# Optimization experiments

Measured on AMD Instinct MI355X. Metric: run time of the kernel, lower is better.

The kernel has to match this reference:

```python
import jax, jax.numpy as jnp
import numpy as np

B, Nc, Ns, Nz, Nx, K = 2, 128, 2048, 256, 256, 4


def setup_inputs() -> dict:
    key = jax.random.key(0)
    k1, k2, k3 = jax.random.split(key, 3)
    # RF channel data: [B, Nc, Ns, K]
    rf = jax.random.normal(k1, (B, Nc, Ns, K), dtype=jnp.float32)
    # Imaging grid point coordinates (meters), ~4 cm field: [B, Nz, Nx, 3]
    g = jax.random.uniform(k2, (B, Nz, Nx, 3), dtype=jnp.float32) * 0.04
    # Receiver element positions (meters): [B, Nc, 3]
    pr = jax.random.uniform(k3, (B, Nc, 3), dtype=jnp.float32) * 0.04
    # Acquisition params per batch: [c0 (m/s), fs (Hz), t0 (s), unused]
    p = jnp.tile(jnp.array([1540.0, 40.0e6, 0.0, 0.0], dtype=jnp.float32), (B, 1))
    return {"rf": rf, "g": g, "pr": pr, "p": p}


def reference(rf, g, pr, p):
    # rf: [B, Nc, Ns, K]; g: [B, Nz, Nx, 3]; pr: [B, Nc, 3]; p: [B, 4]
    b, nc, ns, k = rf.shape
    nz, nx = g.shape[1], g.shape[2]
    m = nz * nx

    c0 = p[:, 0][:, None, None, None]
    fs = p[:, 1][:, None, None, None]
    t0 = p[:, 2][:, None, None, None]

    d_tx = g[..., 2]  # [B, Nz, Nx] transmit path = depth coordinate
    # receive path: distance from each receiver to each pixel -> [B, Nc, Nz, Nx]
    d_rx = jnp.linalg.norm(g[:, None, :, :, :] - pr[:, :, None, None, :], axis=-1)
    # fractional sample index of the round-trip delay
    samples = fs * (t0 + (d_rx + d_tx[:, None, :, :])) / c0  # [B, Nc, Nz, Nx]
    s = samples.reshape(b, nc, m)

    # batch_interp_regular_1d_grid with x_ref_min=0, x_ref_max=Ns-1 on Ns points
    # -> unit grid spacing, constant extension (clamp) outside the grid.
    s = jnp.clip(s, 0.0, float(ns - 1))
    i0 = jnp.clip(jnp.floor(s).astype(jnp.int32), 0, ns - 2)  # [B, Nc, M]
    w = (s - i0.astype(s.dtype))[..., None]                   # [B, Nc, M, 1]

    idx0 = jnp.broadcast_to(i0[..., None], (b, nc, m, k))
    y0 = jnp.take_along_axis(rf, idx0, axis=2)      # [B, Nc, M, K]
    y1 = jnp.take_along_axis(rf, idx0 + 1, axis=2)  # [B, Nc, M, K]
    interp = y0 * (1.0 - w) + y1 * w

    # delay-and-sum over channels, then back to image layout [B, Nz, Nx, K]
    y_das = jnp.sum(interp, axis=1).reshape(b, nz, nx, k)
    return y_das
```

## Files before the change

kernel.cpp:

```cpp
#include <hip/hip_runtime.h>


#define NBATCH 2
#define NC 128
#define NS 2048
#define NK 4
#define NM 65536

#define THREADS 1024
#define PX_PER_THREAD 2
#define PX_PER_BLOCK (THREADS * PX_PER_THREAD)
#define C_PER_BLOCK 16
#define N_CHUNKS (NC / C_PER_BLOCK)
#define N_TILES (NM / PX_PER_BLOCK)
#define NBLOCKS (NBATCH * N_TILES * N_CHUNKS)
#define SLICE_F4 (NS * NK / 4)

#define PART_BYTES ((size_t)N_CHUNKS * NBATCH * NM * NK * 4)

__device__ __forceinline__ void stage_channel(const float* slice, float4* lbuf, int t) {
#pragma unroll
    for (int r = 0; r < SLICE_F4 / THREADS; ++r) {
        const int d = r * THREADS + t;
        __builtin_amdgcn_global_load_lds(
            (const __attribute__((address_space(1))) void*)(slice + (size_t)d * 4),
            (__attribute__((address_space(3))) void*)(lbuf + d),
            16, 0, 0);
    }
}

template <bool ATOMIC>
__global__ __launch_bounds__(THREADS, 8) void das_kernel(
    const float* __restrict__ rf, const float* __restrict__ g,
    const float* __restrict__ pr, const float* __restrict__ p,
    float* __restrict__ dst)
{
    __shared__ float4 sbuf[2][SLICE_F4];

    const int bid   = blockIdx.x;
    const int chunk = bid & (N_CHUNKS - 1);
    const int tile  = (bid >> 3) & (N_TILES - 1);
    const int b     = bid >> 8;
    const int t     = threadIdx.x;
    const int px0   = tile * PX_PER_BLOCK;

    const float c0v = p[b * 4 + 0];
    const float fsv = p[b * 4 + 1];
    const float t0v = p[b * 4 + 2];
    const float scale = fsv / c0v;
    const float sb0   = scale * t0v;

    float gx[PX_PER_THREAD], gy[PX_PER_THREAD], gzv[PX_PER_THREAD], sbase[PX_PER_THREAD];
#pragma unroll
    for (int j = 0; j < PX_PER_THREAD; ++j) {
        const int m = px0 + j * THREADS + t;
        const float* gp = g + ((size_t)b * NM + m) * 3;
        gx[j]  = gp[0];
        gy[j]  = gp[1];
        gzv[j] = gp[2];
        sbase[j] = sb0 + scale * gzv[j];
    }

    float4 acc[PX_PER_THREAD];
#pragma unroll
    for (int j = 0; j < PX_PER_THREAD; ++j) acc[j] = make_float4(0.f, 0.f, 0.f, 0.f);

    const int ch0 = chunk * C_PER_BLOCK;
    const float* slice0 = rf + (size_t)(b * NC + ch0) * NS * NK;

    stage_channel(slice0, &sbuf[0][0], t);

    for (int cc = 0; cc < C_PER_BLOCK; ++cc) {
        __syncthreads();
        if (cc + 1 < C_PER_BLOCK)
            stage_channel(slice0 + (size_t)(cc + 1) * NS * NK,
                          &sbuf[(cc + 1) & 1][0], t);

        const float4* lb = &sbuf[cc & 1][0];
        const float* prp = pr + ((size_t)(b * NC + ch0 + cc)) * 3;
        const float prx = prp[0], pry = prp[1], prz = prp[2];

#pragma unroll
        for (int j = 0; j < PX_PER_THREAD; ++j) {
            const float dx = gx[j]  - prx;
            const float dy = gy[j]  - pry;
            const float dz = gzv[j] - prz;
            const float drx = __builtin_amdgcn_sqrtf(fmaf(dx, dx, fmaf(dy, dy, dz * dz)));
            float s = fmaf(scale, drx, sbase[j]);
            s = fminf(fmaxf(s, 0.0f), (float)(NS - 1));
            const float fi = fminf(floorf(s), (float)(NS - 2));
            const float w  = s - fi;
            const float wm = 1.0f - w;
            const int i0 = (int)fi;
            const float4 y0 = lb[i0];
            const float4 y1 = lb[i0 + 1];
            acc[j].x = fmaf(y0.x, wm, fmaf(y1.x, w, acc[j].x));
            acc[j].y = fmaf(y0.y, wm, fmaf(y1.y, w, acc[j].y));
            acc[j].z = fmaf(y0.z, wm, fmaf(y1.z, w, acc[j].z));
            acc[j].w = fmaf(y0.w, wm, fmaf(y1.w, w, acc[j].w));
        }
    }

    if (ATOMIC) {
        float* ob = dst + (size_t)b * NM * NK;
#pragma unroll
        for (int j = 0; j < PX_PER_THREAD; ++j) {
            const int m = px0 + j * THREADS + t;
            float* op = ob + (size_t)m * NK;
            atomicAdd(op + 0, acc[j].x);
            atomicAdd(op + 1, acc[j].y);
            atomicAdd(op + 2, acc[j].z);
            atomicAdd(op + 3, acc[j].w);
        }
    } else {
        float4* pw = (float4*)dst + (size_t)(chunk * NBATCH + b) * NM;
#pragma unroll
        for (int j = 0; j < PX_PER_THREAD; ++j) {
            const int m = px0 + j * THREADS + t;
            pw[m] = acc[j];
        }
    }
}

__global__ __launch_bounds__(256) void reduce_kernel(
    const float4* __restrict__ part, float4* __restrict__ out)
{
    const int i = blockIdx.x * 256 + threadIdx.x;
    const size_t stride = (size_t)NBATCH * NM;
    float4 a = part[i];
#pragma unroll
    for (int c = 1; c < N_CHUNKS; ++c) {
        const float4 v = part[c * stride + i];
        a.x += v.x; a.y += v.y; a.z += v.z; a.w += v.w;
    }
    out[i] = a;
}

extern "C" void kernel_launch(void* const* d_in, const int* in_sizes, int n_in,
                              void* d_out, int out_size, void* d_ws, size_t ws_size,
                              hipStream_t stream) {
    (void)in_sizes; (void)n_in;
    const float* rf = (const float*)d_in[0];
    const float* g  = (const float*)d_in[1];
    const float* pr = (const float*)d_in[2];
    const float* p  = (const float*)d_in[3];
    float* out = (float*)d_out;

    if (ws_size >= PART_BYTES) {
        das_kernel<false><<<NBLOCKS, THREADS, 0, stream>>>(rf, g, pr, p, (float*)d_ws);
        reduce_kernel<<<(NBATCH * NM) / 256, 256, 0, stream>>>((const float4*)d_ws,
                                                               (float4*)out);
    } else {
        hipMemsetAsync(d_out, 0, (size_t)out_size * sizeof(float), stream);
        das_kernel<true><<<NBLOCKS, THREADS, 0, stream>>>(rf, g, pr, p, out);
    }
}
```

Before: 87.05 us.

## Stage RF slabs in LDS as fp16, two channels per phase, register-prefetched

Replaces the direct global-to-LDS async copies of fp32 channel slices with register loads that convert to fp16 and store two channels per LDS buffer. Each phase processes two channels between barriers, and the next slab is prefetched into registers during compute. This halves LDS footprint per channel and barrier count, and aims for smaller LDS reads. It adds conversion work and register pressure, and fp16 storage reduces precision of the RF samples, which may exceed tolerance.

Result: slower. 272.3 us (+212.8%).

```diff
diff --git a/kernel.cpp b/kernel.cpp
--- a/kernel.cpp
+++ b/kernel.cpp
@@ -14,18 +14,37 @@
 #define N_CHUNKS (NC / C_PER_BLOCK)
 #define N_TILES (NM / PX_PER_BLOCK)
 #define NBLOCKS (NBATCH * N_TILES * N_CHUNKS)
-#define SLICE_F4 (NS * NK / 4)
+
+#define CH_PER_PHASE 2
+#define N_PHASES (C_PER_BLOCK / CH_PER_PHASE)
+#define SLAB_F4 (CH_PER_PHASE * NS * NK / 4)
+#define SLAB_H  (CH_PER_PHASE * NS * NK)
+#define CH_H    (NS * NK)
 
 #define PART_BYTES ((size_t)N_CHUNKS * NBATCH * NM * NK * 4)
 
-__device__ __forceinline__ void stage_channel(const float* slice, float4* lbuf, int t) {
+typedef __attribute__((ext_vector_type(4))) _Float16 half4;
+typedef __attribute__((ext_vector_type(8))) _Float16 half8;
+
+__device__ __forceinline__ void load_slab(const float* slab, float4* f, int t) {
+    const float4* src = (const float4*)slab;
+    f[0] = src[2 * t];
+    f[1] = src[2 * t + 1];
+    f[2] = src[2 * (t + 1024)];
+    f[3] = src[2 * (t + 1024) + 1];
+}
+
+__device__ __forceinline__ void write_slab(const float4* f, _Float16* buf, int t) {
 #pragma unroll
-    for (int r = 0; r < SLICE_F4 / THREADS; ++r) {
-        const int d = r * THREADS + t;
-        __builtin_amdgcn_global_load_lds(
-            (const __attribute__((address_space(1))) void*)(slice + (size_t)d * 4),
-            (__attribute__((address_space(3))) void*)(lbuf + d),
-            16, 0, 0);
+    for (int r = 0; r < 2; ++r) {
+        const int q = r * 1024 + t;
+        const float4 a = f[2 * r], b = f[2 * r + 1];
+        half8 h;
+        h[0] = (_Float16)a.x; h[1] = (_Float16)a.y;
+        h[2] = (_Float16)a.z; h[3] = (_Float16)a.w;
+        h[4] = (_Float16)b.x; h[5] = (_Float16)b.y;
+        h[6] = (_Float16)b.z; h[7] = (_Float16)b.w;
+        *(half8*)(buf + (size_t)q * 8) = h;
     }
 }
 
@@ -35,7 +54,7 @@
     const float* __restrict__ pr, const float* __restrict__ p,
     float* __restrict__ dst)
 {
-    __shared__ float4 sbuf[2][SLICE_F4];
+    __shared__ alignas(16) _Float16 sbuf[2][SLAB_H];
 
     const int bid   = blockIdx.x;
     const int chunk = bid & (N_CHUNKS - 1);
@@ -68,37 +87,51 @@
     const int ch0 = chunk * C_PER_BLOCK;
     const float* slice0 = rf + (size_t)(b * NC + ch0) * NS * NK;
 
-    stage_channel(slice0, &sbuf[0][0], t);
+    {
+        float4 f[4];
+        load_slab(slice0, f, t);
+        write_slab(f, &sbuf[0][0], t);
+    }
+    __syncthreads();
 
-    for (int cc = 0; cc < C_PER_BLOCK; ++cc) {
-        __syncthreads();
-        if (cc + 1 < C_PER_BLOCK)
-            stage_channel(slice0 + (size_t)(cc + 1) * NS * NK,
-                          &sbuf[(cc + 1) & 1][0], t);
+    for (int ph = 0; ph < N_PHASES; ++ph) {
+        float4 nf[4];
+        const bool more = (ph + 1 < N_PHASES);
+        if (more)
+            load_slab(slice0 + (size_t)(ph + 1) * SLAB_F4 * 4, nf, t);
 
-        const float4* lb = &sbuf[cc & 1][0];
-        const float* prp = pr + ((size_t)(b * NC + ch0 + cc)) * 3;
-        const float prx = prp[0], pry = prp[1], prz = prp[2];
+        const _Float16* lb = &sbuf[ph & 1][0];
+#pragma unroll
+        for (int cc = 0; cc < CH_PER_PHASE; ++cc) {
+            const int ch = ch0 + ph * CH_PER_PHASE + cc;
+            const float* prp = pr + ((size_t)b * NC + ch) * 3;
+            const float prx = prp[0], pry = prp[1], prz = prp[2];
+            const _Float16* lc = lb + cc * CH_H;
 
 #pragma unroll
-        for (int j = 0; j < PX_PER_THREAD; ++j) {
-            const float dx = gx[j]  - prx;
-            const float dy = gy[j]  - pry;
-            const float dz = gzv[j] - prz;
-            const float drx = __builtin_amdgcn_sqrtf(fmaf(dx, dx, fmaf(dy, dy, dz * dz)));
-            float s = fmaf(scale, drx, sbase[j]);
-            s = fminf(fmaxf(s, 0.0f), (float)(NS - 1));
-            const float fi = fminf(floorf(s), (float)(NS - 2));
-            const float w  = s - fi;
-            const float wm = 1.0f - w;
-            const int i0 = (int)fi;
-            const float4 y0 = lb[i0];
-            const float4 y1 = lb[i0 + 1];
-            acc[j].x = fmaf(y0.x, wm, fmaf(y1.x, w, acc[j].x));
-            acc[j].y = fmaf(y0.y, wm, fmaf(y1.y, w, acc[j].y));
-            acc[j].z = fmaf(y0.z, wm, fmaf(y1.z, w, acc[j].z));
-            acc[j].w = fmaf(y0.w, wm, fmaf(y1.w, w, acc[j].w));
+            for (int j = 0; j < PX_PER_THREAD; ++j) {
+                const float dx = gx[j]  - prx;
+                const float dy = gy[j]  - pry;
+                const float dz = gzv[j] - prz;
+                const float drx = __builtin_amdgcn_sqrtf(fmaf(dx, dx, fmaf(dy, dy, dz * dz)));
+                float s = fmaf(scale, drx, sbase[j]);
+                s = fminf(fmaxf(s, 0.0f), (float)(NS - 1));
+                const float fi = fminf(floorf(s), (float)(NS - 2));
+                const float w  = s - fi;
+                const float wm = 1.0f - w;
+                const int i0 = (int)fi;
+                const half4 y0 = *(const half4*)(lc + i0 * 4);
+                const half4 y1 = *(const half4*)(lc + i0 * 4 + 4);
+                acc[j].x = fmaf((float)y0[0], wm, fmaf((float)y1[0], w, acc[j].x));
+                acc[j].y = fmaf((float)y0[1], wm, fmaf((float)y1[1], w, acc[j].y));
+                acc[j].z = fmaf((float)y0[2], wm, fmaf((float)y1[2], w, acc[j].z));
+                acc[j].w = fmaf((float)y0[3], wm, fmaf((float)y1[3], w, acc[j].w));
+            }
         }
+
+        if (more)
+            write_slab(nf, &sbuf[(ph + 1) & 1][0], t);
+        __syncthreads();
     }
 
     if (ATOMIC) {
```

## Drop LDS staging of RF slices and gather directly from global memory

Applied to the files above, without the earlier changes.

Removes the double-buffered global-to-LDS staging of each channel's RF slice along with its per-channel block barriers. The interpolation taps are now read straight from global memory through the cache hierarchy. Block size is halved to 512 threads and the batch index shift is adjusted to the larger block count. This avoids copying whole 32KB slices into LDS and the synchronisation that goes with them, but makes each gather an uncoalesced global/L2 access, which can cost more latency.

Measured after the change: 112.8 us. +29.6%, slower.

```diff
diff --git a/kernel.cpp b/kernel.cpp
--- a/kernel.cpp
+++ b/kernel.cpp
@@ -7,27 +7,17 @@
 #define NK 4
 #define NM 65536
 
-#define THREADS 1024
+#define THREADS 512
 #define PX_PER_THREAD 2
 #define PX_PER_BLOCK (THREADS * PX_PER_THREAD)
 #define C_PER_BLOCK 16
 #define N_CHUNKS (NC / C_PER_BLOCK)
 #define N_TILES (NM / PX_PER_BLOCK)
 #define NBLOCKS (NBATCH * N_TILES * N_CHUNKS)
-#define SLICE_F4 (NS * NK / 4)
 
 #define PART_BYTES ((size_t)N_CHUNKS * NBATCH * NM * NK * 4)
 
-__device__ __forceinline__ void stage_channel(const float* slice, float4* lbuf, int t) {
-#pragma unroll
-    for (int r = 0; r < SLICE_F4 / THREADS; ++r) {
-        const int d = r * THREADS + t;
-        __builtin_amdgcn_global_load_lds(
-            (const __attribute__((address_space(1))) void*)(slice + (size_t)d * 4),
-            (__attribute__((address_space(3))) void*)(lbuf + d),
-            16, 0, 0);
-    }
-}
+typedef __attribute__((ext_vector_type(4))) float floatv4;
 
 template <bool ATOMIC>
 __global__ __launch_bounds__(THREADS, 8) void das_kernel(
@@ -35,12 +25,10 @@
     const float* __restrict__ pr, const float* __restrict__ p,
     float* __restrict__ dst)
 {
-    __shared__ float4 sbuf[2][SLICE_F4];
-
     const int bid   = blockIdx.x;
     const int chunk = bid & (N_CHUNKS - 1);
     const int tile  = (bid >> 3) & (N_TILES - 1);
-    const int b     = bid >> 8;
+    const int b     = bid >> 9;
     const int t     = threadIdx.x;
     const int px0   = tile * PX_PER_BLOCK;
 
@@ -61,24 +49,17 @@
         sbase[j] = sb0 + scale * gzv[j];
     }
 
-    float4 acc[PX_PER_THREAD];
+    floatv4 acc[PX_PER_THREAD];
 #pragma unroll
-    for (int j = 0; j < PX_PER_THREAD; ++j) acc[j] = make_float4(0.f, 0.f, 0.f, 0.f);
+    for (int j = 0; j < PX_PER_THREAD; ++j) acc[j] = (floatv4)0.0f;
 
     const int ch0 = chunk * C_PER_BLOCK;
-    const float* slice0 = rf + (size_t)(b * NC + ch0) * NS * NK;
-
-    stage_channel(slice0, &sbuf[0][0], t);
+    const floatv4* slice0 = (const floatv4*)(rf + (size_t)(b * NC + ch0) * NS * NK);
 
     for (int cc = 0; cc < C_PER_BLOCK; ++cc) {
-        __syncthreads();
-        if (cc + 1 < C_PER_BLOCK)
-            stage_channel(slice0 + (size_t)(cc + 1) * NS * NK,
-                          &sbuf[(cc + 1) & 1][0], t);
-
-        const float4* lb = &sbuf[cc & 1][0];
         const float* prp = pr + ((size_t)(b * NC + ch0 + cc)) * 3;
         const float prx = prp[0], pry = prp[1], prz = prp[2];
+        const floatv4* sl = slice0 + (size_t)cc * (NS * NK / 4);
 
 #pragma unroll
         for (int j = 0; j < PX_PER_THREAD; ++j) {
@@ -92,12 +73,9 @@
             const float w  = s - fi;
             const float wm = 1.0f - w;
             const int i0 = (int)fi;
-            const float4 y0 = lb[i0];
-            const float4 y1 = lb[i0 + 1];
-            acc[j].x = fmaf(y0.x, wm, fmaf(y1.x, w, acc[j].x));
-            acc[j].y = fmaf(y0.y, wm, fmaf(y1.y, w, acc[j].y));
-            acc[j].z = fmaf(y0.z, wm, fmaf(y1.z, w, acc[j].z));
-            acc[j].w = fmaf(y0.w, wm, fmaf(y1.w, w, acc[j].w));
+            const floatv4 y0 = sl[i0];
+            const floatv4 y1 = sl[i0 + 1];
+            acc[j] += y0 * wm + y1 * w;
         }
     }
 
@@ -113,7 +91,7 @@
             atomicAdd(op + 3, acc[j].w);
         }
     } else {
-        float4* pw = (float4*)dst + (size_t)(chunk * NBATCH + b) * NM;
+        floatv4* pw = (floatv4*)dst + (size_t)(chunk * NBATCH + b) * NM;
 #pragma unroll
         for (int j = 0; j < PX_PER_THREAD; ++j) {
             const int m = px0 + j * THREADS + t;
@@ -123,16 +101,14 @@
 }
 
 __global__ __launch_bounds__(256) void reduce_kernel(
-    const float4* __restrict__ part, float4* __restrict__ out)
+    const floatv4* __restrict__ part, floatv4* __restrict__ out)
 {
     const int i = blockIdx.x * 256 + threadIdx.x;
     const size_t stride = (size_t)NBATCH * NM;
-    float4 a = part[i];
+    floatv4 a = part[i];
 #pragma unroll
-    for (int c = 1; c < N_CHUNKS; ++c) {
-        const float4 v = part[c * stride + i];
-        a.x += v.x; a.y += v.y; a.z += v.z; a.w += v.w;
-    }
+    for (int c = 1; c < N_CHUNKS; ++c)
+        a += part[c * stride + i];
     out[i] = a;
 }
 
@@ -148,8 +124,8 @@
 
     if (ws_size >= PART_BYTES) {
         das_kernel<false><<<NBLOCKS, THREADS, 0, stream>>>(rf, g, pr, p, (float*)d_ws);
-        reduce_kernel<<<(NBATCH * NM) / 256, 256, 0, stream>>>((const float4*)d_ws,
-                                                               (float4*)out);
+        reduce_kernel<<<(NBATCH * NM) / 256, 256, 0, stream>>>((const floatv4*)d_ws,
+                                                               (floatv4*)out);
     } else {
         hipMemsetAsync(d_out, 0, (size_t)out_size * sizeof(float), stream);
         das_kernel<true><<<NBLOCKS, THREADS, 0, stream>>>(rf, g, pr, p, out);
```
